# Kernel optimization log

Hardware: AMD Instinct MI355X
Metric: run time of the kernel (lower is better)

Reference implementation:

```python
import jax, jax.numpy as jnp
import numpy as np

N = 50000      # nodes
E = 800000     # edges (avg degree 16)
IN_DIM = 256
HID_DIM = 256
OUT_DIM = 64


def _init_linear(key, d_in, d_out):
    # torch nn.Linear default init: U(-1/sqrt(fan_in), 1/sqrt(fan_in))
    s = 1.0 / np.sqrt(d_in)
    kw, kb = jax.random.split(key)
    W = jax.random.uniform(kw, (d_in, d_out), jnp.float32, -s, s)
    b = jax.random.uniform(kb, (d_out,), jnp.float32, -s, s)
    return W, b


def setup_inputs() -> dict:
    key = jax.random.key(0)
    ks = jax.random.split(key, 8)
    x = jax.random.normal(ks[0], (N, IN_DIM), dtype=jnp.float32)
    edge_index = jax.random.randint(ks[1], (2, E), 0, N, dtype=jnp.int64)
    dims = [(IN_DIM, HID_DIM), (HID_DIM, HID_DIM), (HID_DIM, OUT_DIM)]
    out = {"x": x, "edge_index": edge_index}
    for i, (di, do) in enumerate(dims):
        Wl, b = _init_linear(ks[2 + 2 * i], di, do)      # lin_l (on aggregated), with bias
        s = 1.0 / np.sqrt(di)
        Wr = jax.random.uniform(ks[3 + 2 * i], (di, do), jnp.float32, -s, s)  # lin_r (root), no bias
        out[f"Wl{i}"] = Wl
        out[f"Wr{i}"] = Wr
        out[f"b{i}"] = b
    return out


def sage_conv(x, src, dst, Wl, Wr, b):
    # PyG SAGEConv with mean aggregation:
    # out = lin_l(mean_{j in N(i)} x_j) + lin_r(x_i)
    n = x.shape[0]
    msg = x[src]                                              # [E, d] gather
    agg_sum = jax.ops.segment_sum(msg, dst, num_segments=n)   # [N, d] scatter-add
    deg = jax.ops.segment_sum(jnp.ones((src.shape[0], 1), x.dtype), dst, num_segments=n)
    agg = agg_sum / jnp.maximum(deg, 1.0)                     # mean, safe for isolated nodes
    return agg @ Wl + x @ Wr + b


def reference(x, edge_index, Wl0, Wr0, b0, Wl1, Wr1, b1, Wl2, Wr2, b2):
    src, dst = edge_index[0], edge_index[1]
    # dropout is identity in eval mode
    h = jax.nn.relu(sage_conv(x, src, dst, Wl0, Wr0, b0))
    h = jax.nn.relu(sage_conv(h, src, dst, Wl1, Wr1, b1))
    return sage_conv(h, src, dst, Wl2, Wr2, b2)
```

## Files before the change

kernel.cpp:

```cpp
#include <hip/hip_runtime.h>


typedef short bf16x8 __attribute__((ext_vector_type(8)));
typedef float f32x4 __attribute__((ext_vector_type(4)));

__device__ __forceinline__ unsigned short f2bf(float f) {
    unsigned int b = __float_as_uint(f);
    b += 0x7fffu + ((b >> 16) & 1u);
    return (unsigned short)(b >> 16);
}
__device__ __forceinline__ float bflo(unsigned int u) { return __uint_as_float(u << 16); }
__device__ __forceinline__ float bfhi(unsigned int u) { return __uint_as_float(u & 0xffff0000u); }

__device__ __forceinline__ void gload_lds16(const void* g, void* l) {
    __builtin_amdgcn_global_load_lds(
        (const __attribute__((address_space(1))) void*)g,
        (__attribute__((address_space(3))) void*)l, 16, 0, 0);
}

__global__ void fill_pos_kernel(const int* __restrict__ ei, int* __restrict__ cursor,
                                int* __restrict__ pos, int E) {
    int e = blockIdx.x * blockDim.x + threadIdx.x;
    if (e < E) pos[e] = atomicAdd(&cursor[ei[E + e]], 1);
}

__global__ __launch_bounds__(1024) void scan1_kernel(
        const int* __restrict__ deg, int* __restrict__ incl, int* __restrict__ bsum, int n) {
    __shared__ int wsum[16];
    __shared__ int woff[16];
    const int tid = threadIdx.x, lane = tid & 63, wid = tid >> 6;
    int i = blockIdx.x * 1024 + tid;
    int x = (i < n) ? deg[i] : 0;
    #pragma unroll
    for (int off = 1; off < 64; off <<= 1) {
        int t = __shfl_up(x, off, 64);
        if (lane >= off) x += t;
    }
    if (lane == 63) wsum[wid] = x;
    __syncthreads();
    if (tid == 0) {
        int s = 0;
        #pragma unroll
        for (int w = 0; w < 16; ++w) { woff[w] = s; s += wsum[w]; }
        bsum[blockIdx.x] = s;
    }
    __syncthreads();
    if (i < n) incl[i] = x + woff[wid];
}

__global__ void scan2_kernel(int* __restrict__ bsum, int nb) {
    int lane = threadIdx.x;
    int v = (lane < nb) ? bsum[lane] : 0;
    int x = v;
    #pragma unroll
    for (int off = 1; off < 64; off <<= 1) {
        int t = __shfl_up(x, off, 64);
        if (lane >= off) x += t;
    }
    if (lane < nb) bsum[lane] = x - v;
}

__global__ void scan3_kernel(const int* __restrict__ incl, const int* __restrict__ bsum,
                             int* __restrict__ row_ptr, int n) {
    int i = blockIdx.x * blockDim.x + threadIdx.x;
    if (i == 0) row_ptr[0] = 0;
    if (i < n) row_ptr[i + 1] = incl[i] + bsum[i >> 10];
}

__global__ void fill_scatter_kernel(const int* __restrict__ ei, const int* __restrict__ pos,
                                    const int* __restrict__ row_ptr, int* __restrict__ col, int E) {
    int e = blockIdx.x * blockDim.x + threadIdx.x;
    if (e < E) {
        int d = ei[E + e];
        col[row_ptr[d] + pos[e]] = ei[e];
    }
}

__global__ void cvt_bf16_kernel(const float* __restrict__ x, unsigned short* __restrict__ y, int n4) {
    int i = blockIdx.x * blockDim.x + threadIdx.x;
    if (i < n4) {
        float4 v = ((const float4*)x)[i];
        ushort4 o;
        o.x = f2bf(v.x); o.y = f2bf(v.y); o.z = f2bf(v.z); o.w = f2bf(v.w);
        ((ushort4*)y)[i] = o;
    }
}

__global__ void build_bt_kernel(const float* __restrict__ Wl, const float* __restrict__ Wr,
                                unsigned short* __restrict__ BT, int N) {
    int id = blockIdx.x * blockDim.x + threadIdx.x;
    if (id >= N * 512) return;
    int k = id / N;
    int n = id - k * N;
    float v = (k < 256) ? Wl[(size_t)k * N + n] : Wr[(size_t)(k - 256) * N + n];
    BT[(size_t)n * 512 + k] = f2bf(v);
}

__global__ void build_bt1_kernel(const float* __restrict__ W, unsigned short* __restrict__ BT, int N) {
    int id = blockIdx.x * blockDim.x + threadIdx.x;
    if (id >= N * 256) return;
    int k = id / N;
    int n = id - k * N;
    BT[(size_t)n * 256 + k] = f2bf(W[(size_t)k * N + n]);
}

__global__ __launch_bounds__(256) void aggregate256_kernel(
        const unsigned short* __restrict__ h, const int* __restrict__ row_ptr,
        const int* __restrict__ col, unsigned short* __restrict__ agg, int n) {
    int node = blockIdx.x * 4 + (threadIdx.x >> 6);
    int lane = threadIdx.x & 63;
    if (node >= n) return;
    const int start = row_ptr[node], end = row_ptr[node + 1];
    const int half = lane >> 5;
    const int fo = (lane & 31) * 8;
    float a[8] = {0.f, 0.f, 0.f, 0.f, 0.f, 0.f, 0.f, 0.f};
    int eb = start;
    for (; eb + 4 <= end; eb += 4) {
        int e0 = eb + half, e1 = eb + 2 + half;
        uint4 v0 = *(const uint4*)(h + (size_t)col[e0] * 256 + fo);
        uint4 v1 = *(const uint4*)(h + (size_t)col[e1] * 256 + fo);
        a[0] += bflo(v0.x) + bflo(v1.x); a[1] += bfhi(v0.x) + bfhi(v1.x);
        a[2] += bflo(v0.y) + bflo(v1.y); a[3] += bfhi(v0.y) + bfhi(v1.y);
        a[4] += bflo(v0.z) + bflo(v1.z); a[5] += bfhi(v0.z) + bfhi(v1.z);
        a[6] += bflo(v0.w) + bflo(v1.w); a[7] += bfhi(v0.w) + bfhi(v1.w);
    }
    for (; eb < end; eb += 2) {
        int e = eb + half;
        if (e < end) {
            uint4 v = *(const uint4*)(h + (size_t)col[e] * 256 + fo);
            a[0] += bflo(v.x); a[1] += bfhi(v.x);
            a[2] += bflo(v.y); a[3] += bfhi(v.y);
            a[4] += bflo(v.z); a[5] += bfhi(v.z);
            a[6] += bflo(v.w); a[7] += bfhi(v.w);
        }
    }
    #pragma unroll
    for (int i = 0; i < 8; ++i) a[i] += __shfl_xor(a[i], 32, 64);
    int d = end - start;
    float inv = 1.0f / (float)(d > 1 ? d : 1);
    if (lane < 32) {
        ushort4 o0, o1;
        o0.x = f2bf(a[0] * inv); o0.y = f2bf(a[1] * inv);
        o0.z = f2bf(a[2] * inv); o0.w = f2bf(a[3] * inv);
        o1.x = f2bf(a[4] * inv); o1.y = f2bf(a[5] * inv);
        o1.z = f2bf(a[6] * inv); o1.w = f2bf(a[7] * inv);
        *(ushort4*)(agg + (size_t)node * 256 + fo) = o0;
        *(ushort4*)(agg + (size_t)node * 256 + fo + 4) = o1;
    }
}

__global__ __launch_bounds__(256) void aggregate64_kernel(
        const unsigned short* __restrict__ p, const int* __restrict__ row_ptr,
        const int* __restrict__ col, float* __restrict__ aggp, int n) {
    int node = blockIdx.x * 4 + (threadIdx.x >> 6);
    int lane = threadIdx.x & 63;
    if (node >= n) return;
    const int start = row_ptr[node], end = row_ptr[node + 1];
    const int g = lane >> 4;
    const int fo = (lane & 15) * 4;
    float a0 = 0.f, a1 = 0.f, a2 = 0.f, a3 = 0.f;
    int eb = start;
    for (; eb + 8 <= end; eb += 8) {
        int e0 = eb + g, e1 = eb + 4 + g;
        uint2 v0 = *(const uint2*)(p + (size_t)col[e0] * 64 + fo);
        uint2 v1 = *(const uint2*)(p + (size_t)col[e1] * 64 + fo);
        a0 += bflo(v0.x) + bflo(v1.x); a1 += bfhi(v0.x) + bfhi(v1.x);
        a2 += bflo(v0.y) + bflo(v1.y); a3 += bfhi(v0.y) + bfhi(v1.y);
    }
    for (; eb < end; eb += 4) {
        int e = eb + g;
        if (e < end) {
            uint2 v = *(const uint2*)(p + (size_t)col[e] * 64 + fo);
            a0 += bflo(v.x); a1 += bfhi(v.x);
            a2 += bflo(v.y); a3 += bfhi(v.y);
        }
    }
    #pragma unroll
    for (int m = 16; m <= 32; m <<= 1) {
        a0 += __shfl_xor(a0, m, 64);
        a1 += __shfl_xor(a1, m, 64);
        a2 += __shfl_xor(a2, m, 64);
        a3 += __shfl_xor(a3, m, 64);
    }
    int d = end - start;
    float inv = 1.0f / (float)(d > 1 ? d : 1);
    if (lane < 16) {
        float4 o = make_float4(a0 * inv, a1 * inv, a2 * inv, a3 * inv);
        *(float4*)(aggp + (size_t)node * 64 + fo) = o;
    }
}

template<int NKS, int NT, bool RELU, bool OUT_BF16, bool HAS_BIAS, bool HAS_ADD>
__global__ __launch_bounds__(256, 2) void gemm_mfma_kernel(
        const unsigned short* __restrict__ A0, const unsigned short* __restrict__ A1,
        const unsigned short* __restrict__ BT, const float* __restrict__ bias,
        const float* __restrict__ add, void* __restrict__ Cout, int M, int Nc) {
    constexpr int BN = NT * 32;
    constexpr int KB = NKS * 32;
    __shared__ unsigned short As[128 * 32];
    __shared__ unsigned short Bs[BN * 32];
    const int tid = threadIdx.x;
    const int lane = tid & 63;
    const int wid = tid >> 6;
    const int wr = wid >> 1, wc = wid & 1;
    const int row0 = blockIdx.x * 128;
    const int col0 = blockIdx.y * BN;

    f32x4 acc[4][NT];
    #pragma unroll
    for (int i = 0; i < 4; ++i)
        #pragma unroll
        for (int j = 0; j < NT; ++j) acc[i][j] = (f32x4){0.f, 0.f, 0.f, 0.f};

    const int rA = tid >> 2;
    const int kc = (tid & 3) * 8;

    for (int ks = 0; ks < NKS; ++ks) {
        const unsigned short* Asrc = (NKS == 16) ? (ks < 8 ? A0 : A1) : A0;
        const int ka = (NKS == 16) ? ((ks & 7) * 32) : (ks * 32);
        #pragma unroll
        for (int i = 0; i < 2; ++i) {
            const unsigned short* g = Asrc + (size_t)(row0 + rA + i * 64) * 256 + ka + kc;
            gload_lds16(g, As + (size_t)i * 2048 + tid * 8);
        }
        #pragma unroll
        for (int i = 0; i < NT / 2; ++i) {
            const unsigned short* g = BT + (size_t)(col0 + rA + i * 64) * KB + ks * 32 + kc;
            gload_lds16(g, Bs + (size_t)i * 2048 + tid * 8);
        }
        __syncthreads();

        bf16x8 a[4], b[NT];
        #pragma unroll
        for (int tm = 0; tm < 4; ++tm)
            a[tm] = *(const bf16x8*)&As[(wr * 64 + tm * 16 + (lane & 15)) * 32 + (lane >> 4) * 8];
        #pragma unroll
        for (int tn = 0; tn < NT; ++tn)
            b[tn] = *(const bf16x8*)&Bs[(wc * NT * 16 + tn * 16 + (lane & 15)) * 32 + (lane >> 4) * 8];
        #pragma unroll
        for (int tm = 0; tm < 4; ++tm)
            #pragma unroll
            for (int tn = 0; tn < NT; ++tn)
                acc[tm][tn] = __builtin_amdgcn_mfma_f32_16x16x32_bf16(a[tm], b[tn], acc[tm][tn], 0, 0, 0);
        __syncthreads();
    }

    const int cb = col0 + wc * NT * 16;
    #pragma unroll
    for (int tn = 0; tn < NT; ++tn) {
        int colg = cb + tn * 16 + (lane & 15);
        float bv = HAS_BIAS ? bias[colg] : 0.f;
        #pragma unroll
        for (int tm = 0; tm < 4; ++tm) {
            #pragma unroll
            for (int r = 0; r < 4; ++r) {
                int row = row0 + wr * 64 + tm * 16 + (lane >> 4) * 4 + r;
                if (row < M) {
                    float v = acc[tm][tn][r] + bv;
                    if (HAS_ADD) v += add[(size_t)row * Nc + colg];
                    if (RELU) v = fmaxf(v, 0.f);
                    if (OUT_BF16)
                        ((unsigned short*)Cout)[(size_t)row * Nc + colg] = f2bf(v);
                    else
                        ((float*)Cout)[(size_t)row * Nc + colg] = v;
                }
            }
        }
    }
}

extern "C" void kernel_launch(void* const* d_in, const int* in_sizes, int n_in,
                              void* d_out, int out_size, void* d_ws, size_t ws_size,
                              hipStream_t stream) {
    const float* x   = (const float*)d_in[0];
    const int*   ei  = (const int*)d_in[1];
    const float* Wl0 = (const float*)d_in[2];
    const float* Wr0 = (const float*)d_in[3];
    const float* b0  = (const float*)d_in[4];
    const float* Wl1 = (const float*)d_in[5];
    const float* Wr1 = (const float*)d_in[6];
    const float* b1  = (const float*)d_in[7];
    const float* Wl2 = (const float*)d_in[8];
    const float* Wr2 = (const float*)d_in[9];
    const float* b2  = (const float*)d_in[10];
    float* out = (float*)d_out;

    const int Nn = in_sizes[0] / 256;
    const int E  = in_sizes[1] / 2;
    const int Mpad = ((Nn + 127) / 128) * 128;
    const int nb = (Nn + 1023) / 1024;

    char* ws = (char*)d_ws;
    size_t off = 0;
    auto take = [&](size_t bytes) -> void* {
        void* p = (void*)(ws + off);
        off += (bytes + 255) & ~(size_t)255;
        return p;
    };
    int* cursor  = (int*)take((size_t)Nn * 4);
    int* incl    = (int*)take((size_t)Nn * 4);
    int* bsum    = (int*)take((size_t)64 * 4);
    int* row_ptr = (int*)take((size_t)(Nn + 1) * 4);
    int* col     = (int*)take((size_t)E * 4);
    int* pos     = (int*)take((size_t)E * 4);
    unsigned short* xb  = (unsigned short*)take((size_t)Mpad * 256 * 2);
    unsigned short* h1  = (unsigned short*)take((size_t)Mpad * 256 * 2);
    unsigned short* h2  = (unsigned short*)take((size_t)Mpad * 256 * 2);
    unsigned short* h3  = (unsigned short*)take((size_t)Mpad * 256 * 2);
    unsigned short* p2  = (unsigned short*)take((size_t)Mpad * 64 * 2);
    float* aggp = (float*)take((size_t)Mpad * 64 * 4);
    unsigned short* BT0  = (unsigned short*)take((size_t)256 * 512 * 2);
    unsigned short* BT1  = (unsigned short*)take((size_t)256 * 512 * 2);
    unsigned short* BT2l = (unsigned short*)take((size_t)64 * 256 * 2);
    unsigned short* BT2r = (unsigned short*)take((size_t)64 * 256 * 2);
    (void)ws_size; (void)n_in; (void)out_size;

    hipMemsetAsync(cursor, 0, (size_t)Nn * 4, stream);
    fill_pos_kernel<<<(E + 255) / 256, 256, 0, stream>>>(ei, cursor, pos, E);
    scan1_kernel<<<nb, 1024, 0, stream>>>(cursor, incl, bsum, Nn);
    scan2_kernel<<<1, 64, 0, stream>>>(bsum, nb);
    scan3_kernel<<<(Nn + 255) / 256, 256, 0, stream>>>(incl, bsum, row_ptr, Nn);
    fill_scatter_kernel<<<(E + 255) / 256, 256, 0, stream>>>(ei, pos, row_ptr, col, E);

    cvt_bf16_kernel<<<(Nn * 64 + 255) / 256, 256, 0, stream>>>(x, xb, Nn * 64);
    build_bt_kernel<<<(256 * 512 + 255) / 256, 256, 0, stream>>>(Wl0, Wr0, BT0, 256);
    build_bt_kernel<<<(256 * 512 + 255) / 256, 256, 0, stream>>>(Wl1, Wr1, BT1, 256);
    build_bt1_kernel<<<(64 * 256 + 255) / 256, 256, 0, stream>>>(Wl2, BT2l, 64);
    build_bt1_kernel<<<(64 * 256 + 255) / 256, 256, 0, stream>>>(Wr2, BT2r, 64);

    const int gx = Mpad / 128;
    const int aggGrid = (Nn + 3) / 4;

    aggregate256_kernel<<<aggGrid, 256, 0, stream>>>(xb, row_ptr, col, h1, Nn);
    gemm_mfma_kernel<16, 8, true, true, true, false><<<dim3(gx, 1), 256, 0, stream>>>(
        h1, xb, BT0, b0, nullptr, h2, Nn, 256);
    aggregate256_kernel<<<aggGrid, 256, 0, stream>>>(h2, row_ptr, col, h1, Nn);
    gemm_mfma_kernel<16, 8, true, true, true, false><<<dim3(gx, 1), 256, 0, stream>>>(
        h1, h2, BT1, b1, nullptr, h3, Nn, 256);
    gemm_mfma_kernel<8, 2, false, true, false, false><<<dim3(gx, 1), 256, 0, stream>>>(
        h3, nullptr, BT2l, nullptr, nullptr, p2, Nn, 64);
    aggregate64_kernel<<<aggGrid, 256, 0, stream>>>(p2, row_ptr, col, aggp, Nn);
    gemm_mfma_kernel<8, 2, false, false, true, true><<<dim3(gx, 1), 256, 0, stream>>>(
        h3, nullptr, BT2r, b2, aggp, out, Nn, 64);
}
```

Before: 318.4 us.

## Fuse last-layer GEMMs, merge prep kernels, fold scan2 into scan3

Replaces the two separate last-layer GEMMs with a single dual-output kernel. It reads h3 once and produces both the bf16 projection for aggregation and the fp32 root term plus bias directly into the output. The aggregation then accumulates its mean into that output, so the intermediate aggp buffer and its extra pass go away. The bf16 conversion and the four weight-transpose kernels are merged into one prep launch, and the block-sum scan is folded into scan3, which cuts several launches. The trade-off is a read-modify-write on the output and a redundant per-block reduction of block sums in scan3.

```diff
diff --git a/kernel.cpp b/kernel.cpp
--- a/kernel.cpp
+++ b/kernel.cpp
@@ -48,23 +48,21 @@
     if (i < n) incl[i] = x + woff[wid];
 }
 
-__global__ void scan2_kernel(int* __restrict__ bsum, int nb) {
-    int lane = threadIdx.x;
-    int v = (lane < nb) ? bsum[lane] : 0;
-    int x = v;
-    #pragma unroll
-    for (int off = 1; off < 64; off <<= 1) {
-        int t = __shfl_up(x, off, 64);
-        if (lane >= off) x += t;
-    }
-    if (lane < nb) bsum[lane] = x - v;
-}
-
 __global__ void scan3_kernel(const int* __restrict__ incl, const int* __restrict__ bsum,
-                             int* __restrict__ row_ptr, int n) {
-    int i = blockIdx.x * blockDim.x + threadIdx.x;
+                             int* __restrict__ row_ptr, int n, int nb) {
+    __shared__ int off_s;
+    const int chunk = blockIdx.x >> 2;
+    if (threadIdx.x < 64) {
+        int lane = threadIdx.x;
+        int v = (lane < chunk && lane < nb) ? bsum[lane] : 0;
+        #pragma unroll
+        for (int m = 1; m < 64; m <<= 1) v += __shfl_xor(v, m, 64);
+        if (lane == 0) off_s = v;
+    }
+    __syncthreads();
+    int i = blockIdx.x * 256 + threadIdx.x;
     if (i == 0) row_ptr[0] = 0;
-    if (i < n) row_ptr[i + 1] = incl[i] + bsum[i >> 10];
+    if (i < n) row_ptr[i + 1] = incl[i] + off_s;
 }
 
 __global__ void fill_scatter_kernel(const int* __restrict__ ei, const int* __restrict__ pos,
@@ -76,32 +74,47 @@
     }
 }
 
-__global__ void cvt_bf16_kernel(const float* __restrict__ x, unsigned short* __restrict__ y, int n4) {
-    int i = blockIdx.x * blockDim.x + threadIdx.x;
-    if (i < n4) {
-        float4 v = ((const float4*)x)[i];
+__global__ void prep_kernel(const float* __restrict__ x, unsigned short* __restrict__ xb,
+                            const float* __restrict__ Wl0, const float* __restrict__ Wr0,
+                            unsigned short* __restrict__ BT0,
+                            const float* __restrict__ Wl1, const float* __restrict__ Wr1,
+                            unsigned short* __restrict__ BT1,
+                            const float* __restrict__ Wl2, unsigned short* __restrict__ BT2l,
+                            const float* __restrict__ Wr2, unsigned short* __restrict__ BT2r,
+                            int n4) {
+    int t = blockIdx.x * blockDim.x + threadIdx.x;
+    if (t < n4) {
+        float4 v = ((const float4*)x)[t];
         ushort4 o;
         o.x = f2bf(v.x); o.y = f2bf(v.y); o.z = f2bf(v.z); o.w = f2bf(v.w);
-        ((ushort4*)y)[i] = o;
-    }
-}
-
-__global__ void build_bt_kernel(const float* __restrict__ Wl, const float* __restrict__ Wr,
-                                unsigned short* __restrict__ BT, int N) {
-    int id = blockIdx.x * blockDim.x + threadIdx.x;
-    if (id >= N * 512) return;
-    int k = id / N;
-    int n = id - k * N;
-    float v = (k < 256) ? Wl[(size_t)k * N + n] : Wr[(size_t)(k - 256) * N + n];
-    BT[(size_t)n * 512 + k] = f2bf(v);
-}
-
-__global__ void build_bt1_kernel(const float* __restrict__ W, unsigned short* __restrict__ BT, int N) {
-    int id = blockIdx.x * blockDim.x + threadIdx.x;
-    if (id >= N * 256) return;
-    int k = id / N;
-    int n = id - k * N;
-    BT[(size_t)n * 256 + k] = f2bf(W[(size_t)k * N + n]);
+        ((ushort4*)xb)[t] = o;
+        return;
+    }
+    t -= n4;
+    if (t < 131072) {
+        int k = t >> 8, n = t & 255;
+        float v = (k < 256) ? Wl0[(size_t)k * 256 + n] : Wr0[(size_t)(k - 256) * 256 + n];
+        BT0[(size_t)n * 512 + k] = f2bf(v);
+        return;
+    }
+    t -= 131072;
+    if (t < 131072) {
+        int k = t >> 8, n = t & 255;
+        float v = (k < 256) ? Wl1[(size_t)k * 256 + n] : Wr1[(size_t)(k - 256) * 256 + n];
+        BT1[(size_t)n * 512 + k] = f2bf(v);
+        return;
+    }
+    t -= 131072;
+    if (t < 16384) {
+        int k = t >> 6, n = t & 63;
+        BT2l[(size_t)n * 256 + k] = f2bf(Wl2[(size_t)k * 64 + n]);
+        return;
+    }
+    t -= 16384;
+    if (t < 16384) {
+        int k = t >> 6, n = t & 63;
+        BT2r[(size_t)n * 256 + k] = f2bf(Wr2[(size_t)k * 64 + n]);
+    }
 }
 
 __global__ __launch_bounds__(256) void aggregate256_kernel(
@@ -149,9 +162,9 @@
     }
 }
 
-__global__ __launch_bounds__(256) void aggregate64_kernel(
+__global__ __launch_bounds__(256) void agg64_add_kernel(
         const unsigned short* __restrict__ p, const int* __restrict__ row_ptr,
-        const int* __restrict__ col, float* __restrict__ aggp, int n) {
+        const int* __restrict__ col, float* __restrict__ out, int n) {
     int node = blockIdx.x * 4 + (threadIdx.x >> 6);
     int lane = threadIdx.x & 63;
     if (node >= n) return;
@@ -185,16 +198,19 @@
     int d = end - start;
     float inv = 1.0f / (float)(d > 1 ? d : 1);
     if (lane < 16) {
-        float4 o = make_float4(a0 * inv, a1 * inv, a2 * inv, a3 * inv);
-        *(float4*)(aggp + (size_t)node * 64 + fo) = o;
-    }
-}
-
-template<int NKS, int NT, bool RELU, bool OUT_BF16, bool HAS_BIAS, bool HAS_ADD>
+        float* dst = out + (size_t)node * 64 + fo;
+        float4 base = *(float4*)dst;
+        float4 o = make_float4(base.x + a0 * inv, base.y + a1 * inv,
+                               base.z + a2 * inv, base.w + a3 * inv);
+        *(float4*)dst = o;
+    }
+}
+
+template<int NKS, int NT, bool RELU>
 __global__ __launch_bounds__(256, 2) void gemm_mfma_kernel(
         const unsigned short* __restrict__ A0, const unsigned short* __restrict__ A1,
         const unsigned short* __restrict__ BT, const float* __restrict__ bias,
-        const float* __restrict__ add, void* __restrict__ Cout, int M, int Nc) {
+        unsigned short* __restrict__ Cout, int M, int Nc) {
     constexpr int BN = NT * 32;
     constexpr int KB = NKS * 32;
     __shared__ unsigned short As[128 * 32];
@@ -216,8 +232,8 @@
     const int kc = (tid & 3) * 8;
 
     for (int ks = 0; ks < NKS; ++ks) {
-        const unsigned short* Asrc = (NKS == 16) ? (ks < 8 ? A0 : A1) : A0;
-        const int ka = (NKS == 16) ? ((ks & 7) * 32) : (ks * 32);
+        const unsigned short* Asrc = (ks < 8) ? A0 : A1;
+        const int ka = (ks & 7) * 32;
         #pragma unroll
         for (int i = 0; i < 2; ++i) {
             const unsigned short* g = Asrc + (size_t)(row0 + rA + i * 64) * 256 + ka + kc;
@@ -249,7 +265,7 @@
     #pragma unroll
     for (int tn = 0; tn < NT; ++tn) {
         int colg = cb + tn * 16 + (lane & 15);
-        float bv = HAS_BIAS ? bias[colg] : 0.f;
+        float bv = bias[colg];
         #pragma unroll
         for (int tm = 0; tm < 4; ++tm) {
             #pragma unroll
@@ -257,12 +273,85 @@
                 int row = row0 + wr * 64 + tm * 16 + (lane >> 4) * 4 + r;
                 if (row < M) {
                     float v = acc[tm][tn][r] + bv;
-                    if (HAS_ADD) v += add[(size_t)row * Nc + colg];
                     if (RELU) v = fmaxf(v, 0.f);
-                    if (OUT_BF16)
-                        ((unsigned short*)Cout)[(size_t)row * Nc + colg] = f2bf(v);
-                    else
-                        ((float*)Cout)[(size_t)row * Nc + colg] = v;
+                    Cout[(size_t)row * Nc + colg] = f2bf(v);
+                }
+            }
+        }
+    }
+}
+
+__global__ __launch_bounds__(256, 2) void gemm2_dual_kernel(
+        const unsigned short* __restrict__ A,
+        const unsigned short* __restrict__ BTl,
+        const unsigned short* __restrict__ BTr,
+        const float* __restrict__ bias,
+        unsigned short* __restrict__ P2,
+        float* __restrict__ Out, int M) {
+    __shared__ unsigned short As[128 * 32];
+    __shared__ unsigned short Bl[64 * 32];
+    __shared__ unsigned short Br[64 * 32];
+    const int tid = threadIdx.x;
+    const int lane = tid & 63;
+    const int wid = tid >> 6;
+    const int wr = wid >> 1, wc = wid & 1;
+    const int row0 = blockIdx.x * 128;
+
+    f32x4 accL[4][2], accR[4][2];
+    #pragma unroll
+    for (int i = 0; i < 4; ++i)
+        #pragma unroll
+        for (int j = 0; j < 2; ++j) {
+            accL[i][j] = (f32x4){0.f, 0.f, 0.f, 0.f};
+            accR[i][j] = (f32x4){0.f, 0.f, 0.f, 0.f};
+        }
+
+    const int rA = tid >> 2;
+    const int kc = (tid & 3) * 8;
+
+    for (int ks = 0; ks < 8; ++ks) {
+        const int ka = ks * 32;
+        #pragma unroll
+        for (int i = 0; i < 2; ++i) {
+            const unsigned short* g = A + (size_t)(row0 + rA + i * 64) * 256 + ka + kc;
+            gload_lds16(g, As + (size_t)i * 2048 + tid * 8);
+        }
+        gload_lds16(BTl + (size_t)rA * 256 + ka + kc, Bl + tid * 8);
+        gload_lds16(BTr + (size_t)rA * 256 + ka + kc, Br + tid * 8);
+        __syncthreads();
+
+        bf16x8 a[4], bl[2], br[2];
+        #pragma unroll
+        for (int tm = 0; tm < 4; ++tm)
+            a[tm] = *(const bf16x8*)&As[(wr * 64 + tm * 16 + (lane & 15)) * 32 + (lane >> 4) * 8];
+        #pragma unroll
+        for (int tn = 0; tn < 2; ++tn) {
+            int bi = (wc * 32 + tn * 16 + (lane & 15)) * 32 + (lane >> 4) * 8;
+            bl[tn] = *(const bf16x8*)&Bl[bi];
+            br[tn] = *(const bf16x8*)&Br[bi];
+        }
+        #pragma unroll
+        for (int tm = 0; tm < 4; ++tm)
+            #pragma unroll
+            for (int tn = 0; tn < 2; ++tn) {
+                accL[tm][tn] = __builtin_amdgcn_mfma_f32_16x16x32_bf16(a[tm], bl[tn], accL[tm][tn], 0, 0, 0);
+                accR[tm][tn] = __builtin_amdgcn_mfma_f32_16x16x32_bf16(a[tm], br[tn], accR[tm][tn], 0, 0, 0);
+            }
+        __syncthreads();
+    }
+
+    #pragma unroll
+    for (int tn = 0; tn < 2; ++tn) {
+        int colg = wc * 32 + tn * 16 + (lane & 15);
+        float bv = bias[colg];
+        #pragma unroll
+        for (int tm = 0; tm < 4; ++tm) {
+            #pragma unroll
+            for (int r = 0; r < 4; ++r) {
+                int row = row0 + wr * 64 + tm * 16 + (lane >> 4) * 4 + r;
+                if (row < M) {
+                    P2[(size_t)row * 64 + colg] = f2bf(accL[tm][tn][r]);
+                    Out[(size_t)row * 64 + colg] = accR[tm][tn][r] + bv;
                 }
             }
         }
@@ -308,7 +397,6 @@
     unsigned short* h2  = (unsigned short*)take((size_t)Mpad * 256 * 2);
     unsigned short* h3  = (unsigned short*)take((size_t)Mpad * 256 * 2);
     unsigned short* p2  = (unsigned short*)take((size_t)Mpad * 64 * 2);
-    float* aggp = (float*)take((size_t)Mpad * 64 * 4);
     unsigned short* BT0  = (unsigned short*)take((size_t)256 * 512 * 2);
     unsigned short* BT1  = (unsigned short*)take((size_t)256 * 512 * 2);
     unsigned short* BT2l = (unsigned short*)take((size_t)64 * 256 * 2);
@@ -318,28 +406,23 @@
     hipMemsetAsync(cursor, 0, (size_t)Nn * 4, stream);
     fill_pos_kernel<<<(E + 255) / 256, 256, 0, stream>>>(ei, cursor, pos, E);
     scan1_kernel<<<nb, 1024, 0, stream>>>(cursor, incl, bsum, Nn);
-    scan2_kernel<<<1, 64, 0, stream>>>(bsum, nb);
-    scan3_kernel<<<(Nn + 255) / 256, 256, 0, stream>>>(incl, bsum, row_ptr, Nn);
+    scan3_kernel<<<(Nn + 255) / 256, 256, 0, stream>>>(incl, bsum, row_ptr, Nn, nb);
     fill_scatter_kernel<<<(E + 255) / 256, 256, 0, stream>>>(ei, pos, row_ptr, col, E);
 
-    cvt_bf16_kernel<<<(Nn * 64 + 255) / 256, 256, 0, stream>>>(x, xb, Nn * 64);
-    build_bt_kernel<<<(256 * 512 + 255) / 256, 256, 0, stream>>>(Wl0, Wr0, BT0, 256);
-    build_bt_kernel<<<(256 * 512 + 255) / 256, 256, 0, stream>>>(Wl1, Wr1, BT1, 256);
-    build_bt1_kernel<<<(64 * 256 + 255) / 256, 256, 0, stream>>>(Wl2, BT2l, 64);
-    build_bt1_kernel<<<(64 * 256 + 255) / 256, 256, 0, stream>>>(Wr2, BT2r, 64);
+    const int n4 = Nn * 64;
+    const int prepTot = n4 + 131072 + 131072 + 16384 + 16384;
+    prep_kernel<<<(prepTot + 255) / 256, 256, 0, stream>>>(
+        x, xb, Wl0, Wr0, BT0, Wl1, Wr1, BT1, Wl2, BT2l, Wr2, BT2r, n4);
 
     const int gx = Mpad / 128;
     const int aggGrid = (Nn + 3) / 4;
 
     aggregate256_kernel<<<aggGrid, 256, 0, stream>>>(xb, row_ptr, col, h1, Nn);
-    gemm_mfma_kernel<16, 8, true, true, true, false><<<dim3(gx, 1), 256, 0, stream>>>(
-        h1, xb, BT0, b0, nullptr, h2, Nn, 256);
+    gemm_mfma_kernel<16, 8, true><<<dim3(gx, 1), 256, 0, stream>>>(
+        h1, xb, BT0, b0, h2, Nn, 256);
     aggregate256_kernel<<<aggGrid, 256, 0, stream>>>(h2, row_ptr, col, h1, Nn);
-    gemm_mfma_kernel<16, 8, true, true, true, false><<<dim3(gx, 1), 256, 0, stream>>>(
-        h1, h2, BT1, b1, nullptr, h3, Nn, 256);
-    gemm_mfma_kernel<8, 2, false, true, false, false><<<dim3(gx, 1), 256, 0, stream>>>(
-        h3, nullptr, BT2l, nullptr, nullptr, p2, Nn, 64);
-    aggregate64_kernel<<<aggGrid, 256, 0, stream>>>(p2, row_ptr, col, aggp, Nn);
-    gemm_mfma_kernel<8, 2, false, false, true, true><<<dim3(gx, 1), 256, 0, stream>>>(
-        h3, nullptr, BT2r, b2, aggp, out, Nn, 64);
-}
+    gemm_mfma_kernel<16, 8, true><<<dim3(gx, 1), 256, 0, stream>>>(
+        h1, h2, BT1, b1, h3, Nn, 256);
+    gemm2_dual_kernel<<<gx, 256, 0, stream>>>(h3, BT2l, BT2r, b2, p2, out, Nn);
+    agg64_add_kernel<<<aggGrid, 256, 0, stream>>>(p2, row_ptr, col, out, Nn);
+}
```

Result: faster. 299.8 us (-5.8%).
